# Kernel tuning notes

Hardware: AMD Instinct MI355X
Metric: run time of the kernel (lower is better)

Reference implementation:

```python
import jax, jax.numpy as jnp
import numpy as np

N_EMBD = 1024
N_HEAD = 16
HEAD_SIZE = N_EMBD // N_HEAD  # 64
HEAD_INDEX = 0
# ALiBi slope: x = (2**8)**(1/n_head); slope = 1 / x**(head_index+1)
SLOPE = 1.0 / ((2.0 ** 8) ** (1.0 / N_HEAD)) ** (HEAD_INDEX + 1)
B, T = 4, 4096


def setup_inputs() -> dict:
    key = jax.random.key(0)
    kx, kq, kk, kv = jax.random.split(key, 4)
    x = jax.random.normal(kx, (B, T, N_EMBD), dtype=jnp.float32)
    wq = jax.random.normal(kq, (HEAD_SIZE, N_EMBD), dtype=jnp.float32) * 0.02
    wk = jax.random.normal(kk, (HEAD_SIZE, N_EMBD), dtype=jnp.float32) * 0.02
    wv = jax.random.normal(kv, (HEAD_SIZE, N_EMBD), dtype=jnp.float32) * 0.02
    return {"x": x, "wq": wq, "wk": wk, "wv": wv}


def reference(x, wq, wk, wv):
    Bq, Tq, C = x.shape
    q = jnp.einsum('btc,hc->bth', x, wq)  # [B,T,Hd]
    k = jnp.einsum('btc,hc->bth', x, wk)
    v = jnp.einsum('btc,hc->bth', x, wv)
    # NOTE: original scales by C**-0.5 where C = n_embd (full dim), not head_size
    wei = jnp.einsum('bth,bsh->bts', q, k) * (C ** -0.5)  # [B,T,T]
    idx = jnp.arange(Tq)
    distance = idx[None, :] - idx[:, None]  # [T,T], j - i
    wei = wei + distance.astype(wei.dtype) * jnp.asarray(SLOPE, wei.dtype)
    causal = distance <= 0  # tril: key index j <= query index i
    wei = jnp.where(causal[None, :, :], wei, -jnp.inf)
    wei = jax.nn.softmax(wei, axis=-1)
    out = jnp.einsum('bts,bsh->bth', wei, v)  # [B,T,Hd]
    return out
```

## Files before the change

### kernel.cpp

```cpp
#include <hip/hip_runtime.h>
#include <hip/hip_bf16.h>
#include <stdint.h>
#include <math.h>

typedef __attribute__((ext_vector_type(8))) short bf16x8;
typedef __attribute__((ext_vector_type(4))) float f32x4;

#define TSEQ 4096
#define LOG2E 1.44269504088896340736f
#define SLOPE 0.70710678118654752440f
#define SL2E (SLOPE * LOG2E)

__device__ __forceinline__ unsigned short f32_to_bf16(float f) {
  union { float f; unsigned int u; } v; v.f = f;
  unsigned int r = v.u + 0x7fffu + ((v.u >> 16) & 1u);
  return (unsigned short)(r >> 16);
}

__device__ __forceinline__ unsigned int pk2(float a, float b) {
  union { __hip_bfloat162 h; unsigned int u; } c;
  c.h = __float22bfloat162_rn(make_float2(a, b));
  return c.u;
}
__device__ __forceinline__ bf16x8 cvt8(f32x4 a, f32x4 b) {
  union { unsigned int u[4]; bf16x8 v; } r;
  r.u[0] = pk2(a[0], a[1]); r.u[1] = pk2(a[2], a[3]);
  r.u[2] = pk2(b[0], b[1]); r.u[3] = pk2(b[2], b[3]);
  return r.v;
}

__device__ __forceinline__ void async_cp16(const void* g, void* l) {
  __builtin_amdgcn_global_load_lds(
      (const __attribute__((address_space(1))) unsigned int*)g,
      (__attribute__((address_space(3))) unsigned int*)l, 16, 0, 0);
}

__global__ __launch_bounds__(256) void init_kernel(
    const float* __restrict__ wq, const float* __restrict__ wk,
    const float* __restrict__ wv, unsigned short* __restrict__ Wb) {
  int tid = blockIdx.x * 256 + threadIdx.x;
  if (tid >= 24576) return;
  int lane = tid & 63, s = (tid >> 6) & 31, nt = (tid >> 11) & 3, t = tid >> 13;
  int n = nt * 16 + (lane & 15);
  int k = s * 32 + (lane >> 4) * 8;
  const float* src = (t == 0 ? wq : (t == 1 ? wk : wv)) + (size_t)n * 1024 + k;
  f32x4 a = *(const f32x4*)src;
  f32x4 b = *(const f32x4*)(src + 4);
  if (t == 0) {
#pragma unroll
    for (int j = 0; j < 4; ++j) { a[j] *= 0.03125f; b[j] *= 0.03125f; }
  }
  *(bf16x8*)(Wb + (size_t)tid * 8) = cvt8(a, b);
}

__global__ __launch_bounds__(512, 2) void proj_kernel(
    const float* __restrict__ x, const unsigned short* __restrict__ Wb,
    unsigned short* __restrict__ qb, unsigned short* __restrict__ kb,
    unsigned short* __restrict__ vt) {
  __shared__ float xbuf[3][32][64];

  const int tix = threadIdx.x;
  const int lane = tix & 63;
  const int wave = tix >> 6;
  const int wr = wave >> 2;
  const int wc = wave & 3;
  const int l16 = lane & 15, quad = lane >> 4;
  const int R0 = blockIdx.x * 32;

  f32x4 acc[3];
#pragma unroll
  for (int i = 0; i < 3; ++i) acc[i] = (f32x4){0.f, 0.f, 0.f, 0.f};

  const int srow = wave * 4 + quad;
  const float* xsrc = x + (size_t)(R0 + srow) * 1024 + (l16 ^ (srow & 15)) * 4;

  const unsigned short* wsrc[6];
#pragma unroll
  for (int cc = 0; cc < 3; ++cc)
#pragma unroll
    for (int ss = 0; ss < 2; ++ss)
      wsrc[cc * 2 + ss] = Wb + ((size_t)((wc * 3 + cc) * 32 + ss) * 64 + lane) * 8;

  auto stage_x = [&](int s, int bi) {
    async_cp16(xsrc + s * 64, &xbuf[bi][wave * 4][0]);
  };
  auto load_w = [&](int s, bf16x8 (&w)[6]) {
#pragma unroll
    for (int j = 0; j < 6; ++j)
      w[j] = *(const bf16x8*)(wsrc[j] + (size_t)s * 1024);
  };

  bf16x8 wA[6], wB[6];
  stage_x(0, 0);
  __builtin_amdgcn_sched_barrier(0);
  load_w(0, wA);
  __builtin_amdgcn_sched_barrier(0);
  stage_x(1, 1);
  __builtin_amdgcn_sched_barrier(0);

  auto step_body = [&](int s, bf16x8 (&win)[6], bf16x8 (&wout)[6]) {
    if (s < 15) asm volatile("s_waitcnt vmcnt(1)" ::: "memory");
    else        asm volatile("s_waitcnt vmcnt(0)" ::: "memory");
    __builtin_amdgcn_sched_barrier(0);
    if (s + 1 < 16) load_w(s + 1, wout);
    __builtin_amdgcn_sched_barrier(0);
    __builtin_amdgcn_s_barrier();
    __builtin_amdgcn_sched_barrier(0);
    if (s + 2 < 16) stage_x(s + 2, (s + 2) % 3);
    __builtin_amdgcn_sched_barrier(0);
    const int cur = s % 3;
#pragma unroll
    for (int ss = 0; ss < 2; ++ss) {
      const float* base = &xbuf[cur][wr * 16 + l16][0];
      f32x4 a0 = *(const f32x4*)(base + ((ss * 8 + quad * 2) ^ l16) * 4);
      f32x4 a1 = *(const f32x4*)(base + ((ss * 8 + quad * 2 + 1) ^ l16) * 4);
      bf16x8 af = cvt8(a0, a1);
#pragma unroll
      for (int cc = 0; cc < 3; ++cc)
        acc[cc] = __builtin_amdgcn_mfma_f32_16x16x32_bf16(
            af, win[cc * 2 + ss], acc[cc], 0, 0, 0);
    }
    __builtin_amdgcn_sched_barrier(0);
  };

#pragma unroll 1
  for (int sp = 0; sp < 16; sp += 2) {
    step_body(sp, wA, wB);
    step_body(sp + 1, wB, wA);
  }

#pragma unroll
  for (int cc = 0; cc < 3; ++cc) {
    const int ci = wc * 3 + cc;
#pragma unroll
    for (int r = 0; r < 4; ++r) {
      int row = R0 + wr * 16 + quad * 4 + r;
      unsigned short hv = f32_to_bf16(acc[cc][r]);
      if (ci < 4) {
        qb[(size_t)row * 64 + ci * 16 + l16] = hv;
      } else if (ci < 8) {
        kb[(size_t)row * 64 + (ci - 4) * 16 + l16] = hv;
      } else {
        int b = row >> 12, tt = row & 4095;
        vt[((size_t)b * 64 + (ci - 8) * 16 + l16) * TSEQ + tt] = hv;
      }
    }
  }
}

__global__ __launch_bounds__(64) void attn_kernel(
    const unsigned short* __restrict__ qb, const unsigned short* __restrict__ kb,
    const unsigned short* __restrict__ vt, float* __restrict__ out) {
  __shared__ unsigned short pbuf[16][40];

  const int lane = threadIdx.x & 63;
  const int l16 = lane & 15, quad = lane >> 4;
  const int tid = blockIdx.x;
  const int b = tid & 3;
  const int r0 = (tid >> 2) << 4;
  const int j0 = (r0 >= 16) ? (r0 - 16) : 0;

  const unsigned short* kbase = kb + (size_t)b * TSEQ * 64;
  const unsigned short* vbase = vt + (size_t)b * 64 * TSEQ;

  const unsigned short* qrow = qb + (size_t)(b * TSEQ + r0 + l16) * 64 + quad * 8;
  bf16x8 qa0 = *(const bf16x8*)qrow;
  bf16x8 qa1 = *(const bf16x8*)(qrow + 32);

  f32x4 o[5];
#pragma unroll
  for (int dt = 0; dt < 5; ++dt) o[dt] = (f32x4){0.f, 0.f, 0.f, 0.f};

  const int irel = j0 + l16 - r0 - quad * 4;
  const float fb = SL2E * (float)irel;

#pragma unroll
  for (int nt = 0; nt < 2; ++nt) {
    const unsigned short* krow = kbase + (size_t)(j0 + nt * 16 + l16) * 64 + quad * 8;
    f32x4 sa = (f32x4){0.f, 0.f, 0.f, 0.f};
    sa = __builtin_amdgcn_mfma_f32_16x16x32_bf16(qa0, *(const bf16x8*)krow, sa, 0, 0, 0);
    sa = __builtin_amdgcn_mfma_f32_16x16x32_bf16(qa1, *(const bf16x8*)(krow + 32), sa, 0, 0, 0);
#pragma unroll
    for (int r = 0; r < 4; ++r) {
      float arg = fmaf(sa[r], LOG2E, fb + SL2E * (float)(nt * 16 - r));
      float p = exp2f(arg);
      if (irel + nt * 16 - r > 0) p = 0.f;
      pbuf[quad * 4 + r][nt * 16 + l16] = f32_to_bf16(p);
    }
  }
  bf16x8 pa = *(const bf16x8*)&pbuf[l16][quad * 8];

#pragma unroll
  for (int dt = 0; dt < 4; ++dt) {
    const unsigned short* vrow = vbase + (size_t)(dt * 16 + l16) * TSEQ + j0 + quad * 8;
    o[dt] = __builtin_amdgcn_mfma_f32_16x16x32_bf16(pa, *(const bf16x8*)vrow, o[dt], 0, 0, 0);
  }
  {
    union { unsigned int u[4]; bf16x8 v; } ones;
    ones.u[0] = ones.u[1] = ones.u[2] = ones.u[3] = 0x3F803F80u;
    o[4] = __builtin_amdgcn_mfma_f32_16x16x32_bf16(pa, ones.v, o[4], 0, 0, 0);
  }

#pragma unroll
  for (int r = 0; r < 4; ++r) {
    const float invl = 1.0f / o[4][r];
    const int row = b * TSEQ + r0 + quad * 4 + r;
#pragma unroll
    for (int dt = 0; dt < 4; ++dt)
      out[(size_t)row * 64 + dt * 16 + l16] = o[dt][r] * invl;
  }
}

extern "C" void kernel_launch(void* const* d_in, const int* in_sizes, int n_in,
                              void* d_out, int out_size, void* d_ws, size_t ws_size,
                              hipStream_t stream) {
  const float* x  = (const float*)d_in[0];
  const float* wq = (const float*)d_in[1];
  const float* wk = (const float*)d_in[2];
  const float* wv = (const float*)d_in[3];
  float* out = (float*)d_out;

  char* ws = (char*)d_ws;
  unsigned short* Wb = (unsigned short*)(ws);
  unsigned short* qb = (unsigned short*)(ws + 393216);
  unsigned short* kb = (unsigned short*)(ws + 393216 + 2097152);
  unsigned short* vt = (unsigned short*)(ws + 393216 + 2 * 2097152);

  init_kernel<<<96, 256, 0, stream>>>(wq, wk, wv, Wb);
  proj_kernel<<<512, 512, 0, stream>>>(x, Wb, qb, kb, vt);
  attn_kernel<<<1024, 64, 0, stream>>>(qb, kb, vt, out);
}
```

Baseline: 124.5 us.

## Restructure projection kernel into per-wave private x tiles without block barriers

```diff
diff --git a/kernel.cpp b/kernel.cpp
--- a/kernel.cpp
+++ b/kernel.cpp
@@ -57,81 +57,72 @@
     const float* __restrict__ x, const unsigned short* __restrict__ Wb,
     unsigned short* __restrict__ qb, unsigned short* __restrict__ kb,
     unsigned short* __restrict__ vt) {
-  __shared__ float xbuf[3][32][64];
+  __shared__ float xb[8][2][16][64];
 
   const int tix = threadIdx.x;
   const int lane = tix & 63;
   const int wave = tix >> 6;
-  const int wr = wave >> 2;
-  const int wc = wave & 3;
+  const int wr = wave >> 1;
+  const int wc = wave & 1;
   const int l16 = lane & 15, quad = lane >> 4;
-  const int R0 = blockIdx.x * 32;
-
-  f32x4 acc[3];
-#pragma unroll
-  for (int i = 0; i < 3; ++i) acc[i] = (f32x4){0.f, 0.f, 0.f, 0.f};
-
-  const int srow = wave * 4 + quad;
-  const float* xsrc = x + (size_t)(R0 + srow) * 1024 + (l16 ^ (srow & 15)) * 4;
-
+  const int R0 = blockIdx.x * 64;
+
+  f32x4 acc[6];
+#pragma unroll
+  for (int i = 0; i < 6; ++i) acc[i] = (f32x4){0.f, 0.f, 0.f, 0.f};
+
+  const float* xsrc[4];
+#pragma unroll
+  for (int c = 0; c < 4; ++c) {
+    int rg = c * 4 + quad;
+    int g = l16 ^ (rg & 15);
+    xsrc[c] = x + (size_t)(R0 + wr * 16 + rg) * 1024 + g * 4;
+  }
   const unsigned short* wsrc[6];
 #pragma unroll
-  for (int cc = 0; cc < 3; ++cc)
-#pragma unroll
-    for (int ss = 0; ss < 2; ++ss)
-      wsrc[cc * 2 + ss] = Wb + ((size_t)((wc * 3 + cc) * 32 + ss) * 64 + lane) * 8;
-
-  auto stage_x = [&](int s, int bi) {
-    async_cp16(xsrc + s * 64, &xbuf[bi][wave * 4][0]);
+  for (int cc = 0; cc < 6; ++cc)
+    wsrc[cc] = Wb + ((size_t)((wc * 6 + cc) * 32) * 64 + lane) * 8;
+
+  auto stage = [&](int s, int bi) {
+#pragma unroll
+    for (int c = 0; c < 4; ++c)
+      async_cp16(xsrc[c] + s * 64, &xb[wave][bi][c * 4][0]);
   };
-  auto load_w = [&](int s, bf16x8 (&w)[6]) {
-#pragma unroll
-    for (int j = 0; j < 6; ++j)
-      w[j] = *(const bf16x8*)(wsrc[j] + (size_t)s * 1024);
-  };
-
-  bf16x8 wA[6], wB[6];
-  stage_x(0, 0);
-  __builtin_amdgcn_sched_barrier(0);
-  load_w(0, wA);
-  __builtin_amdgcn_sched_barrier(0);
-  stage_x(1, 1);
-  __builtin_amdgcn_sched_barrier(0);
-
-  auto step_body = [&](int s, bf16x8 (&win)[6], bf16x8 (&wout)[6]) {
-    if (s < 15) asm volatile("s_waitcnt vmcnt(1)" ::: "memory");
-    else        asm volatile("s_waitcnt vmcnt(0)" ::: "memory");
-    __builtin_amdgcn_sched_barrier(0);
-    if (s + 1 < 16) load_w(s + 1, wout);
-    __builtin_amdgcn_sched_barrier(0);
-    __builtin_amdgcn_s_barrier();
-    __builtin_amdgcn_sched_barrier(0);
-    if (s + 2 < 16) stage_x(s + 2, (s + 2) % 3);
-    __builtin_amdgcn_sched_barrier(0);
-    const int cur = s % 3;
+
+  stage(0, 0);
+
+#pragma unroll 2
+  for (int s = 0; s < 16; ++s) {
+    const int cur = s & 1;
+    bf16x8 w[6][2];
+#pragma unroll
+    for (int cc = 0; cc < 6; ++cc)
+#pragma unroll
+      for (int ss = 0; ss < 2; ++ss)
+        w[cc][ss] = *(const bf16x8*)(wsrc[cc] + (size_t)(2 * s + ss) * 512);
+    __builtin_amdgcn_sched_barrier(0);
+    if (s + 1 < 16) stage(s + 1, 1 - cur);
+    __builtin_amdgcn_sched_barrier(0);
+    if (s + 1 < 16) asm volatile("s_waitcnt vmcnt(4)" ::: "memory");
+    else            asm volatile("s_waitcnt vmcnt(0)" ::: "memory");
+    __builtin_amdgcn_sched_barrier(0);
 #pragma unroll
     for (int ss = 0; ss < 2; ++ss) {
-      const float* base = &xbuf[cur][wr * 16 + l16][0];
+      const float* base = &xb[wave][cur][l16][0];
       f32x4 a0 = *(const f32x4*)(base + ((ss * 8 + quad * 2) ^ l16) * 4);
       f32x4 a1 = *(const f32x4*)(base + ((ss * 8 + quad * 2 + 1) ^ l16) * 4);
       bf16x8 af = cvt8(a0, a1);
 #pragma unroll
-      for (int cc = 0; cc < 3; ++cc)
+      for (int cc = 0; cc < 6; ++cc)
         acc[cc] = __builtin_amdgcn_mfma_f32_16x16x32_bf16(
-            af, win[cc * 2 + ss], acc[cc], 0, 0, 0);
+            af, w[cc][ss], acc[cc], 0, 0, 0);
     }
     __builtin_amdgcn_sched_barrier(0);
-  };
-
-#pragma unroll 1
-  for (int sp = 0; sp < 16; sp += 2) {
-    step_body(sp, wA, wB);
-    step_body(sp + 1, wB, wA);
-  }
-
-#pragma unroll
-  for (int cc = 0; cc < 3; ++cc) {
-    const int ci = wc * 3 + cc;
+  }
+
+#pragma unroll
+  for (int cc = 0; cc < 6; ++cc) {
+    const int ci = wc * 6 + cc;
 #pragma unroll
     for (int r = 0; r < 4; ++r) {
       int row = R0 + wr * 16 + quad * 4 + r;
@@ -227,6 +218,6 @@
   unsigned short* vt = (unsigned short*)(ws + 393216 + 2 * 2097152);
 
   init_kernel<<<96, 256, 0, stream>>>(wq, wk, wv, Wb);
-  proj_kernel<<<512, 512, 0, stream>>>(x, Wb, qb, kb, vt);
+  proj_kernel<<<256, 512, 0, stream>>>(x, Wb, qb, kb, vt);
   attn_kernel<<<1024, 64, 0, stream>>>(qb, kb, vt, out);
 }
```

Result: slower. 128.2 us (+3.0%).
